# Optimization experiments

Measured on AMD Instinct MI355X. Metric: run time of the kernel, lower is better.

Reference implementation:

```python
import jax, jax.numpy as jnp
import numpy as np

B, N, C = 4, 4096, 1024
NUM_HEADS = 16
HEAD_DIM = C // NUM_HEADS


def setup_inputs() -> dict:
    key = jax.random.key(0)
    k1, k2, k3, k4 = jax.random.split(key, 4)
    s_in = 1.0 / np.sqrt(C)
    return {
        "x": jax.random.normal(k1, (B, N, C), dtype=jnp.float32),
        "H": 64,
        "W": 64,
        "Wqkv": jax.random.normal(k2, (3 * C, C), dtype=jnp.float32) * s_in,
        "Wproj": jax.random.normal(k3, (C, C), dtype=jnp.float32) * s_in,
        "bproj": jnp.zeros((C,), dtype=jnp.float32),
        "alpha": jnp.ones((NUM_HEADS,), dtype=jnp.float32),
    }


def reference(x, H, W, Wqkv, Wproj, bproj, alpha):
    Bb, Nn, Cc = x.shape
    h, d = NUM_HEADS, HEAD_DIM
    # qkv: [B, N, 3C] -> [3, B, h, N, d]
    qkv = jnp.einsum('bnc,oc->bno', x, Wqkv)
    qkv = qkv.reshape(Bb, Nn, 3, h, d).transpose(2, 0, 3, 1, 4)
    q, k, v = qkv[0], qkv[1], qkv[2]  # each [B, h, N, d]
    # channel attention: contract over tokens N -> [B, h, d, d]
    attn = jnp.einsum('bhnd,bhne->bhde', k, q) / alpha[None, :, None, None]
    attn = jax.nn.softmax(attn, axis=-1)
    # (dropout is identity in eval/reference mode)
    # head_out: [B, h, d, N] -> transpose -> [B, N, h, d] -> concat heads
    out = jnp.einsum('bhde,bhne->bhdn', attn, v)
    out = out.transpose(0, 3, 1, 2).reshape(Bb, Nn, Cc)
    return jnp.einsum('bnc,oc->bno', out, Wproj) + bproj
```

## Files before the change

### kernel.cpp

```cpp
#include <hip/hip_runtime.h>
#include <hip/hip_bf16.h>
#include <cstdint>
#include <cstddef>

typedef unsigned short u16;
typedef __bf16 bf16x8 __attribute__((ext_vector_type(8)));
typedef float f32x4 __attribute__((ext_vector_type(4)));
typedef unsigned short u16x4 __attribute__((ext_vector_type(4)));

#define AS1(p) ((__attribute__((address_space(1))) void*)(p))
#define AS3(p) ((__attribute__((address_space(3))) void*)(p))

__device__ __forceinline__ float bf2f(u16 u) {
  unsigned v = ((unsigned)u) << 16; float f; __builtin_memcpy(&f, &v, 4); return f;
}
__device__ __forceinline__ u16 f2bf(float f) {
  unsigned u; __builtin_memcpy(&u, &f, 4);
  u += 0x7FFFu + ((u >> 16) & 1u);
  return (u16)(u >> 16);
}

__global__ __launch_bounds__(256) void convert_kernel(const float* __restrict__ src,
                                                      u16* __restrict__ dst, int n4) {
  int i = blockIdx.x * blockDim.x + threadIdx.x;
  int stride = gridDim.x * blockDim.x;
  for (; i < n4; i += stride) {
    float4 v = ((const float4*)src)[i];
    u16x4 o;
    o.x = f2bf(v.x); o.y = f2bf(v.y); o.z = f2bf(v.z); o.w = f2bf(v.w);
    ((u16x4*)dst)[i] = o;
  }
}

__global__ __launch_bounds__(256) void convert_split_kernel(const float* __restrict__ src,
                                                            u16* __restrict__ hi,
                                                            u16* __restrict__ lo, int n4) {
  int i = blockIdx.x * blockDim.x + threadIdx.x;
  int stride = gridDim.x * blockDim.x;
  for (; i < n4; i += stride) {
    float4 v = ((const float4*)src)[i];
    u16x4 oh, ol;
    oh.x = f2bf(v.x); ol.x = f2bf(v.x - bf2f(oh.x));
    oh.y = f2bf(v.y); ol.y = f2bf(v.y - bf2f(oh.y));
    oh.z = f2bf(v.z); ol.z = f2bf(v.z - bf2f(oh.z));
    oh.w = f2bf(v.w); ol.w = f2bf(v.w - bf2f(oh.w));
    ((u16x4*)hi)[i] = oh;
    ((u16x4*)lo)[i] = ol;
  }
}

__global__ __launch_bounds__(256) void transpose_split_kernel(const float* __restrict__ x,
                                                              u16* __restrict__ Xb,
                                                              u16* __restrict__ XThi,
                                                              u16* __restrict__ XTlo) {
  __shared__ u16 lhi[64 * 68];
  __shared__ u16 llo[64 * 68];
  const int t  = threadIdx.x;
  const int nT = blockIdx.x, cT = blockIdx.y, b = blockIdx.z;
  const size_t xbase = ((size_t)b * 4096 + nT * 64) * 1024 + cT * 64;
  const int c4 = (t & 15) * 4;
  const int r0 = t >> 4;
#pragma unroll
  for (int j = 0; j < 4; ++j) {
    int r = r0 + j * 16;
    float4 v = *(const float4*)(x + xbase + (size_t)r * 1024 + c4);
    u16x4 hi;
    hi.x = f2bf(v.x); hi.y = f2bf(v.y); hi.z = f2bf(v.z); hi.w = f2bf(v.w);
    *(u16x4*)(Xb + xbase + (size_t)r * 1024 + c4) = hi;
    u16 lo[4];
    lo[0] = f2bf(v.x - bf2f(hi.x)); lo[1] = f2bf(v.y - bf2f(hi.y));
    lo[2] = f2bf(v.z - bf2f(hi.z)); lo[3] = f2bf(v.w - bf2f(hi.w));
    u16 hia[4] = { hi.x, hi.y, hi.z, hi.w };
#pragma unroll
    for (int i = 0; i < 4; ++i) {
      lhi[(c4 + i) * 68 + r] = hia[i];
      llo[(c4 + i) * 68 + r] = lo[i];
    }
  }
  __syncthreads();
  const int c  = t >> 2;
  const int n0 = (t & 3) * 16;
  const size_t tbase = ((size_t)b * 1024 + cT * 64 + c) * 4096 + nT * 64 + n0;
#pragma unroll
  for (int q = 0; q < 4; ++q) {
    *(u16x4*)(XThi + tbase + q * 4) = *(const u16x4*)(lhi + c * 68 + n0 + q * 4);
    *(u16x4*)(XTlo + tbase + q * 4) = *(const u16x4*)(llo + c * 68 + n0 + q * 4);
  }
}

template<bool OUT_BF16, bool HAS_BIAS>
__global__ __launch_bounds__(256) void gemm_bt(const u16* __restrict__ A,
                                               const u16* __restrict__ B,
                                               void* __restrict__ Cv,
                                               const float* __restrict__ bias,
                                               int M, int N, int K) {
  __shared__ __align__(16) u16 lA[128 * 32];
  __shared__ __align__(16) u16 lB[128 * 32];
  const int tid  = threadIdx.x;
  const int lane = tid & 63;
  const int wave = tid >> 6;
  const int rowTile = blockIdx.x * 128;
  const int colTile = blockIdx.y * 128;
  const int wr = (wave >> 1) * 64;
  const int wc = (wave & 1) * 64;

  f32x4 acc[4][4] = {};
  const int m  = lane & 15;
  const int ko = (lane >> 4) * 8;

  for (int kt = 0; kt < K; kt += 32) {
#pragma unroll
    for (int i = 0; i < 2; ++i) {
      int idx = i * 256 + tid;
      int row = idx >> 2;
      int kc  = (idx & 3) * 8;
      int ldsOff = (i * 256 + (tid & 192)) * 16;
      __builtin_amdgcn_global_load_lds(AS1(A + (size_t)(rowTile + row) * K + kt + kc),
                                       AS3((char*)lA + ldsOff), 16, 0, 0);
      __builtin_amdgcn_global_load_lds(AS1(B + (size_t)(colTile + row) * K + kt + kc),
                                       AS3((char*)lB + ldsOff), 16, 0, 0);
    }
    __syncthreads();
    bf16x8 af[4], bfr[4];
#pragma unroll
    for (int rb = 0; rb < 4; ++rb)
      af[rb] = *(const bf16x8*)(lA + (wr + rb * 16 + m) * 32 + ko);
#pragma unroll
    for (int cb = 0; cb < 4; ++cb)
      bfr[cb] = *(const bf16x8*)(lB + (wc + cb * 16 + m) * 32 + ko);
#pragma unroll
    for (int rb = 0; rb < 4; ++rb)
#pragma unroll
      for (int cb = 0; cb < 4; ++cb)
        acc[rb][cb] = __builtin_amdgcn_mfma_f32_16x16x32_bf16(af[rb], bfr[cb], acc[rb][cb], 0, 0, 0);
    __syncthreads();
  }

  const int crow0 = rowTile + wr + (lane >> 4) * 4;
  const int ccol0 = colTile + wc + (lane & 15);
#pragma unroll
  for (int rb = 0; rb < 4; ++rb) {
#pragma unroll
    for (int cb = 0; cb < 4; ++cb) {
      int col = ccol0 + cb * 16;
      float bv = HAS_BIAS ? bias[col] : 0.f;
#pragma unroll
      for (int r = 0; r < 4; ++r) {
        int row = crow0 + rb * 16 + r;
        float v = acc[rb][cb][r] + bv;
        if (OUT_BF16) ((u16*)Cv)[(size_t)row * N + col] = f2bf(v);
        else          ((float*)Cv)[(size_t)row * N + col] = v;
      }
    }
  }
}

__global__ __launch_bounds__(256) void gemm_vm(const u16* __restrict__ V,
                                               const u16* __restrict__ Mb,
                                               float* __restrict__ Y,
                                               const float* __restrict__ bias) {
  __shared__ __align__(16) u16 lA[128 * 32];
  __shared__ __align__(16) u16 lB[128 * 32];
  const int tid  = threadIdx.x;
  const int lane = tid & 63;
  const int wave = tid >> 6;
  const int rowTile = blockIdx.x * 128;
  const int colTile = blockIdx.y * 128;
  const int bz = blockIdx.z;
  const u16* A = V + ((size_t)bz << 22);
  const u16* B = Mb + ((size_t)bz << 20);
  float* C = Y + ((size_t)bz << 22);
  const int wr = (wave >> 1) * 64;
  const int wc = (wave & 1) * 64;

  f32x4 acc[4][4] = {};
  const int m  = lane & 15;
  const int ko = (lane >> 4) * 8;

  for (int kt = 0; kt < 1024; kt += 32) {
#pragma unroll
    for (int i = 0; i < 2; ++i) {
      int idx = i * 256 + tid;
      int row = idx >> 2;
      int kc  = (idx & 3) * 8;
      int ldsOff = (i * 256 + (tid & 192)) * 16;
      __builtin_amdgcn_global_load_lds(AS1(A + (size_t)(rowTile + row) * 1024 + kt + kc),
                                       AS3((char*)lA + ldsOff), 16, 0, 0);
      __builtin_amdgcn_global_load_lds(AS1(B + (size_t)(colTile + row) * 1024 + kt + kc),
                                       AS3((char*)lB + ldsOff), 16, 0, 0);
    }
    __syncthreads();
    bf16x8 af[4], bfr[4];
#pragma unroll
    for (int rb = 0; rb < 4; ++rb)
      af[rb] = *(const bf16x8*)(lA + (wr + rb * 16 + m) * 32 + ko);
#pragma unroll
    for (int cb = 0; cb < 4; ++cb)
      bfr[cb] = *(const bf16x8*)(lB + (wc + cb * 16 + m) * 32 + ko);
#pragma unroll
    for (int rb = 0; rb < 4; ++rb)
#pragma unroll
      for (int cb = 0; cb < 4; ++cb)
        acc[rb][cb] = __builtin_amdgcn_mfma_f32_16x16x32_bf16(af[rb], bfr[cb], acc[rb][cb], 0, 0, 0);
    __syncthreads();
  }

  const int crow0 = rowTile + wr + (lane >> 4) * 4;
  const int ccol0 = colTile + wc + (lane & 15);
#pragma unroll
  for (int rb = 0; rb < 4; ++rb)
#pragma unroll
    for (int cb = 0; cb < 4; ++cb) {
      int col = ccol0 + cb * 16;
      float bv = bias[col];
#pragma unroll
      for (int r = 0; r < 4; ++r)
        C[(size_t)(crow0 + rb * 16 + r) * 1024 + col] = acc[rb][cb][r] + bv;
    }
}

__global__ __launch_bounds__(256) void gemm_gram(const u16* __restrict__ XThi,
                                                 const u16* __restrict__ XTlo,
                                                 float* __restrict__ Gpart) {
  __shared__ __align__(16) u16 lAh[128 * 32];
  __shared__ __align__(16) u16 lAl[128 * 32];
  __shared__ __align__(16) u16 lBh[128 * 32];
  __shared__ __align__(16) u16 lBl[128 * 32];
  const int tid  = threadIdx.x;
  const int lane = tid & 63;
  const int wave = tid >> 6;
  const int wr = (wave >> 1) * 64;
  const int wc = (wave & 1) * 64;
  const int m  = lane & 15;
  const int ko = (lane >> 4) * 8;

  const int u0 = blockIdx.x * 36;
  const int b  = u0 / 4608;
  int ub   = u0 - b * 4608;
  int tile = ub >> 7;
  int koff = ub & 127;

  const u16* Ahp = XThi + ((size_t)b << 22);
  const u16* Alp = XTlo + ((size_t)b << 22);
  float* out = Gpart + ((size_t)b << 20);

  int remaining = 36;
  for (int seg = 0; seg < 2 && remaining > 0; ++seg) {
    int niter = min(remaining, 128 - koff);
    int t = tile, rt = 0;
    while (t >= 8 - rt) { t -= 8 - rt; ++rt; }
    int ct = rt + t;
    const int rowTile = rt * 128, colTile = ct * 128;

    f32x4 acc[4][4] = {};
    const int kend = (koff + niter) * 32;
    for (int kt = koff * 32; kt < kend; kt += 32) {
#pragma unroll
      for (int i = 0; i < 2; ++i) {
        int idx = i * 256 + tid;
        int row = idx >> 2;
        int kc  = (idx & 3) * 8;
        int ldsOff = (i * 256 + (tid & 192)) * 16;
        size_t aoff = (size_t)(rowTile + row) * 4096 + kt + kc;
        size_t boff = (size_t)(colTile + row) * 4096 + kt + kc;
        __builtin_amdgcn_global_load_lds(AS1(Ahp + aoff), AS3((char*)lAh + ldsOff), 16, 0, 0);
        __builtin_amdgcn_global_load_lds(AS1(Alp + aoff), AS3((char*)lAl + ldsOff), 16, 0, 0);
        __builtin_amdgcn_global_load_lds(AS1(Ahp + boff), AS3((char*)lBh + ldsOff), 16, 0, 0);
        __builtin_amdgcn_global_load_lds(AS1(Alp + boff), AS3((char*)lBl + ldsOff), 16, 0, 0);
      }
      __syncthreads();
      bf16x8 ah[4], al[4], bh[4], bl[4];
#pragma unroll
      for (int rb = 0; rb < 4; ++rb) {
        ah[rb] = *(const bf16x8*)(lAh + (wr + rb * 16 + m) * 32 + ko);
        al[rb] = *(const bf16x8*)(lAl + (wr + rb * 16 + m) * 32 + ko);
      }
#pragma unroll
      for (int cb = 0; cb < 4; ++cb) {
        bh[cb] = *(const bf16x8*)(lBh + (wc + cb * 16 + m) * 32 + ko);
        bl[cb] = *(const bf16x8*)(lBl + (wc + cb * 16 + m) * 32 + ko);
      }
#pragma unroll
      for (int rb = 0; rb < 4; ++rb)
#pragma unroll
        for (int cb = 0; cb < 4; ++cb) {
          acc[rb][cb] = __builtin_amdgcn_mfma_f32_16x16x32_bf16(ah[rb], bh[cb], acc[rb][cb], 0, 0, 0);
          acc[rb][cb] = __builtin_amdgcn_mfma_f32_16x16x32_bf16(ah[rb], bl[cb], acc[rb][cb], 0, 0, 0);
          acc[rb][cb] = __builtin_amdgcn_mfma_f32_16x16x32_bf16(al[rb], bh[cb], acc[rb][cb], 0, 0, 0);
        }
      __syncthreads();
    }

    const int crow0 = rowTile + wr + (lane >> 4) * 4;
    const int ccol0 = colTile + wc + (lane & 15);
#pragma unroll
    for (int rb = 0; rb < 4; ++rb)
#pragma unroll
      for (int cb = 0; cb < 4; ++cb)
#pragma unroll
        for (int r = 0; r < 4; ++r)
          atomicAdd(&out[(size_t)(crow0 + rb * 16 + r) * 1024 + ccol0 + cb * 16],
                    acc[rb][cb][r]);

    remaining -= niter;
    tile += 1;
    koff = 0;
  }
}

__global__ __launch_bounds__(256) void gram_reduce_split(const float* __restrict__ Gp,
                                                         u16* __restrict__ Ghi,
                                                         u16* __restrict__ Glo) {
  const int rt = blockIdx.x, ct = blockIdx.y, b = blockIdx.z;
  const float* P = Gp + ((size_t)b << 20);
  const bool mirror = (rt >> 1) > (ct >> 1);
  __shared__ float lT[64 * 68];
  const int t = threadIdx.x;
  const int r = t >> 2;
  const int c16 = (t & 3) * 16;

  if (mirror) {
    const size_t bb = (size_t)(ct * 64 + r) * 1024 + rt * 64 + c16;
#pragma unroll
    for (int q = 0; q < 4; ++q)
      *(float4*)(lT + r * 68 + c16 + q * 4) = *(const float4*)(P + bb + q * 4);
    __syncthreads();
  }

  const size_t ab = (size_t)(rt * 64 + r) * 1024 + ct * 64 + c16;
  const size_t ob = ((size_t)b << 20) + ab;
#pragma unroll
  for (int q = 0; q < 4; ++q) {
    float g[4];
    if (mirror) {
#pragma unroll
      for (int i = 0; i < 4; ++i) g[i] = lT[(c16 + q * 4 + i) * 68 + r];
    } else {
      float4 v = *(const float4*)(P + ab + q * 4);
      g[0] = v.x; g[1] = v.y; g[2] = v.z; g[3] = v.w;
    }
    u16x4 oh, ol;
    oh.x = f2bf(g[0]); ol.x = f2bf(g[0] - bf2f(oh.x));
    oh.y = f2bf(g[1]); ol.y = f2bf(g[1] - bf2f(oh.y));
    oh.z = f2bf(g[2]); ol.z = f2bf(g[2] - bf2f(oh.z));
    oh.w = f2bf(g[3]); ol.w = f2bf(g[3] - bf2f(oh.w));
    *(u16x4*)(Ghi + ob + q * 4) = oh;
    *(u16x4*)(Glo + ob + q * 4) = ol;
  }
}

__global__ __launch_bounds__(256) void gemm_tprime(const u16* __restrict__ Wqh,
                                                   const u16* __restrict__ Wql,
                                                   const u16* __restrict__ Ghi,
                                                   const u16* __restrict__ Glo,
                                                   u16* __restrict__ Tph,
                                                   u16* __restrict__ Tpl) {
  __shared__ __align__(16) u16 lAh[128 * 32];
  __shared__ __align__(16) u16 lAl[128 * 32];
  __shared__ __align__(16) u16 lBh[128 * 32];
  __shared__ __align__(16) u16 lBl[128 * 32];
  const int tid  = threadIdx.x;
  const int lane = tid & 63;
  const int wave = tid >> 6;
  const int rowTile = blockIdx.x * 128;
  const int colTile = blockIdx.y * 128;
  const size_t zoff = (size_t)blockIdx.z << 20;
  const int wr = (wave >> 1) * 64;
  const int wc = (wave & 1) * 64;

  f32x4 acc[4][4] = {};
  const int m  = lane & 15;
  const int ko = (lane >> 4) * 8;

  for (int kt = 0; kt < 1024; kt += 32) {
#pragma unroll
    for (int i = 0; i < 2; ++i) {
      int idx = i * 256 + tid;
      int row = idx >> 2;
      int kc  = (idx & 3) * 8;
      int ldsOff = (i * 256 + (tid & 192)) * 16;
      size_t aoff = (size_t)(rowTile + row) * 1024 + kt + kc;
      size_t boff = zoff + (size_t)(colTile + row) * 1024 + kt + kc;
      __builtin_amdgcn_global_load_lds(AS1(Wqh + aoff), AS3((char*)lAh + ldsOff), 16, 0, 0);
      __builtin_amdgcn_global_load_lds(AS1(Wql + aoff), AS3((char*)lAl + ldsOff), 16, 0, 0);
      __builtin_amdgcn_global_load_lds(AS1(Ghi + boff), AS3((char*)lBh + ldsOff), 16, 0, 0);
      __builtin_amdgcn_global_load_lds(AS1(Glo + boff), AS3((char*)lBl + ldsOff), 16, 0, 0);
    }
    __syncthreads();
    bf16x8 ah[4], al[4], bh[4], bl[4];
#pragma unroll
    for (int rb = 0; rb < 4; ++rb) {
      ah[rb] = *(const bf16x8*)(lAh + (wr + rb * 16 + m) * 32 + ko);
      al[rb] = *(const bf16x8*)(lAl + (wr + rb * 16 + m) * 32 + ko);
    }
#pragma unroll
    for (int cb = 0; cb < 4; ++cb) {
      bh[cb] = *(const bf16x8*)(lBh + (wc + cb * 16 + m) * 32 + ko);
      bl[cb] = *(const bf16x8*)(lBl + (wc + cb * 16 + m) * 32 + ko);
    }
#pragma unroll
    for (int rb = 0; rb < 4; ++rb)
#pragma unroll
      for (int cb = 0; cb < 4; ++cb) {
        acc[rb][cb] = __builtin_amdgcn_mfma_f32_16x16x32_bf16(ah[rb], bh[cb], acc[rb][cb], 0, 0, 0);
        acc[rb][cb] = __builtin_amdgcn_mfma_f32_16x16x32_bf16(ah[rb], bl[cb], acc[rb][cb], 0, 0, 0);
        acc[rb][cb] = __builtin_amdgcn_mfma_f32_16x16x32_bf16(al[rb], bh[cb], acc[rb][cb], 0, 0, 0);
      }
    __syncthreads();
  }

  const int crow0 = rowTile + wr + (lane >> 4) * 4;
  const int ccol0 = colTile + wc + (lane & 15);
#pragma unroll
  for (int rb = 0; rb < 4; ++rb)
#pragma unroll
    for (int cb = 0; cb < 4; ++cb)
#pragma unroll
      for (int r = 0; r < 4; ++r) {
        float v = acc[rb][cb][r];
        u16 hi = f2bf(v);
        u16 lo = f2bf(v - bf2f(hi));
        size_t off = zoff + (size_t)(crow0 + rb * 16 + r) * 1024 + ccol0 + cb * 16;
        Tph[off] = hi;
        Tpl[off] = lo;
      }
}

__global__ __launch_bounds__(256) void s_softmax_kernel(const u16* __restrict__ Wqh,
                                                        const u16* __restrict__ Wql,
                                                        const u16* __restrict__ Tph,
                                                        const u16* __restrict__ Tpl,
                                                        const float* __restrict__ alpha,
                                                        u16* __restrict__ attnT) {
  const int h = blockIdx.x, b = blockIdx.y;
  const int tid = threadIdx.x, lane = tid & 63, wave = tid >> 6;
  __shared__ __align__(16) u16 lAh[64 * 32];
  __shared__ __align__(16) u16 lAl[64 * 32];
  __shared__ __align__(16) u16 lBh[64 * 32];
  __shared__ __align__(16) u16 lBl[64 * 32];

  const size_t aBase = (size_t)(1024 + h * 64) * 1024;
  const size_t bBase = ((size_t)b << 20) + (size_t)(h * 64) * 1024;

  f32x4 acc[4] = {};
  const int m  = lane & 15;
  const int ko = (lane >> 4) * 8;
  const int srow = tid >> 2;
  const int skc  = (tid & 3) * 8;
  const int ldsOff = (tid & 192) * 16;

  for (int kt = 0; kt < 1024; kt += 32) {
    __builtin_amdgcn_global_load_lds(AS1(Wqh + aBase + (size_t)srow * 1024 + kt + skc),
                                     AS3((char*)lAh + ldsOff), 16, 0, 0);
    __builtin_amdgcn_global_load_lds(AS1(Wql + aBase + (size_t)srow * 1024 + kt + skc),
                                     AS3((char*)lAl + ldsOff), 16, 0, 0);
    __builtin_amdgcn_global_load_lds(AS1(Tph + bBase + (size_t)srow * 1024 + kt + skc),
                                     AS3((char*)lBh + ldsOff), 16, 0, 0);
    __builtin_amdgcn_global_load_lds(AS1(Tpl + bBase + (size_t)srow * 1024 + kt + skc),
                                     AS3((char*)lBl + ldsOff), 16, 0, 0);
    __syncthreads();
    bf16x8 ah = *(const bf16x8*)(lAh + (wave * 16 + m) * 32 + ko);
    bf16x8 al = *(const bf16x8*)(lAl + (wave * 16 + m) * 32 + ko);
#pragma unroll
    for (int cb = 0; cb < 4; ++cb) {
      bf16x8 bh = *(const bf16x8*)(lBh + (cb * 16 + m) * 32 + ko);
      bf16x8 bl = *(const bf16x8*)(lBl + (cb * 16 + m) * 32 + ko);
      acc[cb] = __builtin_amdgcn_mfma_f32_16x16x32_bf16(ah, bh, acc[cb], 0, 0, 0);
      acc[cb] = __builtin_amdgcn_mfma_f32_16x16x32_bf16(ah, bl, acc[cb], 0, 0, 0);
      acc[cb] = __builtin_amdgcn_mfma_f32_16x16x32_bf16(al, bh, acc[cb], 0, 0, 0);
    }
    __syncthreads();
  }

  const float invA = 1.f / alpha[h];
  const int g = lane >> 4;
  const size_t obase = (size_t)(b * 16 + h) * 4096;
#pragma unroll
  for (int r = 0; r < 4; ++r) {
    int d = wave * 16 + g * 4 + r;
    float s[4];
#pragma unroll
    for (int cb = 0; cb < 4; ++cb) s[cb] = acc[cb][r] * invA;
    float mx = fmaxf(fmaxf(s[0], s[1]), fmaxf(s[2], s[3]));
#pragma unroll
    for (int o = 1; o < 16; o <<= 1) mx = fmaxf(mx, __shfl_xor(mx, o, 64));
    float e[4]; float sum = 0.f;
#pragma unroll
    for (int cb = 0; cb < 4; ++cb) { e[cb] = __expf(s[cb] - mx); sum += e[cb]; }
#pragma unroll
    for (int o = 1; o < 16; o <<= 1) sum += __shfl_xor(sum, o, 64);
    float inv = 1.f / sum;
#pragma unroll
    for (int cb = 0; cb < 4; ++cb) {
      int e_idx = cb * 16 + (lane & 15);
      attnT[obase + (size_t)e_idx * 64 + d] = f2bf(e[cb] * inv);
    }
  }
}

__global__ __launch_bounds__(256) void m_build_kernel(const u16* __restrict__ Wpb,
                                                      const u16* __restrict__ attnT,
                                                      u16* __restrict__ Mb) {
  const int oT = blockIdx.x, h = blockIdx.y, b = blockIdx.z;
  const int tid = threadIdx.x, lane = tid & 63, wave = tid >> 6;
  __shared__ __align__(16) u16 lA[128 * 64];
  __shared__ __align__(16) u16 lB[64 * 64];
  const int bh = b * 16 + h;
#pragma unroll
  for (int i = 0; i < 4; ++i) {
    int idx = i * 256 + tid;
    int row = idx >> 3;
    int kc  = (idx & 7) * 8;
    int ldsOff = (i * 256 + (tid & 192)) * 16;
    __builtin_amdgcn_global_load_lds(AS1(Wpb + (size_t)(oT * 128 + row) * 1024 + h * 64 + kc),
                                     AS3((char*)lA + ldsOff), 16, 0, 0);
  }
#pragma unroll
  for (int i = 0; i < 2; ++i) {
    int idx = i * 256 + tid;
    int ldsOff = (i * 256 + (tid & 192)) * 16;
    __builtin_amdgcn_global_load_lds(AS1(attnT + (size_t)bh * 4096 + idx * 8),
                                     AS3((char*)lB + ldsOff), 16, 0, 0);
  }
  __syncthreads();
  const int m  = lane & 15;
  const int ko = (lane >> 4) * 8;
  const int wr = wave * 32;
  f32x4 acc[2][4] = {};
#pragma unroll
  for (int ks = 0; ks < 2; ++ks) {
#pragma unroll
    for (int rb = 0; rb < 2; ++rb) {
      bf16x8 a = *(const bf16x8*)(lA + (wr + rb * 16 + m) * 64 + ks * 32 + ko);
#pragma unroll
      for (int cb = 0; cb < 4; ++cb) {
        bf16x8 bb = *(const bf16x8*)(lB + (cb * 16 + m) * 64 + ks * 32 + ko);
        acc[rb][cb] = __builtin_amdgcn_mfma_f32_16x16x32_bf16(a, bb, acc[rb][cb], 0, 0, 0);
      }
    }
  }
  u16* out = Mb + ((size_t)b << 20);
#pragma unroll
  for (int rb = 0; rb < 2; ++rb)
#pragma unroll
    for (int cb = 0; cb < 4; ++cb) {
      int col = h * 64 + cb * 16 + (lane & 15);
#pragma unroll
      for (int r = 0; r < 4; ++r) {
        int row = oT * 128 + wr + rb * 16 + (lane >> 4) * 4 + r;
        out[(size_t)row * 1024 + col] = f2bf(acc[rb][cb][r]);
      }
    }
}

extern "C" void kernel_launch(void* const* d_in, const int* in_sizes, int n_in,
                              void* d_out, int out_size, void* d_ws, size_t ws_size,
                              hipStream_t stream) {
  const float* x     = (const float*)d_in[0];
  const float* Wqkv  = (const float*)d_in[3];
  const float* Wproj = (const float*)d_in[4];
  const float* bproj = (const float*)d_in[5];
  const float* alpha = (const float*)d_in[6];

  char* ws = (char*)d_ws;
  u16*   Xb     = (u16*)ws;
  float* Gpart  = (float*)ws;
  u16*   Mb     = (u16*)ws;
  u16*   XThi   = (u16*)(ws + 33554432);
  u16*   attnTb = (u16*)(ws + 33554432);
  u16*   XTlo  = (u16*)(ws + 67108864);
  u16*   Ghi   = (u16*)(ws + 67108864);
  u16*   Glo   = (u16*)(ws + 75497472);
  u16*   Tph   = (u16*)(ws + 83886080);
  u16*   Tpl   = (u16*)(ws + 92274688);
  u16*   Wqh   = (u16*)(ws + 100663296);
  u16*   Wql   = (u16*)(ws + 106954752);
  u16*   Vb    = (u16*)(ws + 113246208);
  u16*   Wpb   = (u16*)(ws + 146800640);

  transpose_split_kernel<<<dim3(64, 16, 4), 256, 0, stream>>>(x, Xb, XThi, XTlo);
  convert_split_kernel<<<256, 256, 0, stream>>>(Wqkv, Wqh, Wql, 3145728 / 4);
  convert_kernel<<<128, 256, 0, stream>>>(Wproj, Wpb, 1048576 / 4);
  gemm_bt<true, false><<<dim3(128, 8), 256, 0, stream>>>(
      Xb, Wqh + (size_t)2048 * 1024, Vb, nullptr, 16384, 1024, 1024);
  hipMemsetAsync(Gpart, 0, (size_t)4 * 1024 * 1024 * 4, stream);
  gemm_gram<<<512, 256, 0, stream>>>(XThi, XTlo, Gpart);
  gram_reduce_split<<<dim3(16, 16, 4), 256, 0, stream>>>(Gpart, Ghi, Glo);
  gemm_tprime<<<dim3(8, 8, 4), 256, 0, stream>>>(Wqh, Wql, Ghi, Glo, Tph, Tpl);
  s_softmax_kernel<<<dim3(16, 4), 256, 0, stream>>>(Wqh, Wql, Tph, Tpl, alpha, attnTb);
  m_build_kernel<<<dim3(8, 16, 4), 256, 0, stream>>>(Wpb, attnTb, Mb);
  gemm_vm<<<dim3(32, 8, 4), 256, 0, stream>>>(Vb, Mb, (float*)d_out, bproj);
}
```

Baseline: 458.5 us.

## Restructure Gram GEMM split-K into fixed quarter slices with plain stores

The Gram kernel no longer assigns each block a flat run of 36 k-iterations that may span two tiles. It now uses a 2D grid where each upper-triangle tile is split into four K quarters. For off-diagonal tiles, the two upper quarters are written transposed into the mirror position, so each output location gets plain stores instead of atomics. Diagonal tiles still accumulate with atomics into two slice buffers, and the reduce kernel now sums both slices plus the mirrored transpose. This removes most atomic traffic and the segment bookkeeping, at the cost of a larger memset and extra partial-buffer reads in the reduce.

```diff
diff --git a/kernel.cpp b/kernel.cpp
--- a/kernel.cpp
+++ b/kernel.cpp
@@ -234,65 +234,64 @@
   const int m  = lane & 15;
   const int ko = (lane >> 4) * 8;
 
-  const int u0 = blockIdx.x * 36;
-  const int b  = u0 / 4608;
-  int ub   = u0 - b * 4608;
-  int tile = ub >> 7;
-  int koff = ub & 127;
+  const int jx = blockIdx.x;
+  const int b  = blockIdx.y;
+  const int tile = jx >> 2, kq = jx & 3;
+  int t = tile, rt = 0;
+  while (t >= 8 - rt) { t -= 8 - rt; ++rt; }
+  const int ct = rt + t;
+  const bool diag = (rt == ct);
+  int rT = rt, cT = ct;
+  if (!diag && kq >= 2) { rT = ct; cT = rt; }
+  const int slice = kq & 1;
+  const int rowTile = rT * 128, colTile = cT * 128;
+  const int k0 = kq * 1024;
 
   const u16* Ahp = XThi + ((size_t)b << 22);
   const u16* Alp = XTlo + ((size_t)b << 22);
-  float* out = Gpart + ((size_t)b << 20);
-
-  int remaining = 36;
-  for (int seg = 0; seg < 2 && remaining > 0; ++seg) {
-    int niter = min(remaining, 128 - koff);
-    int t = tile, rt = 0;
-    while (t >= 8 - rt) { t -= 8 - rt; ++rt; }
-    int ct = rt + t;
-    const int rowTile = rt * 128, colTile = ct * 128;
-
-    f32x4 acc[4][4] = {};
-    const int kend = (koff + niter) * 32;
-    for (int kt = koff * 32; kt < kend; kt += 32) {
-#pragma unroll
-      for (int i = 0; i < 2; ++i) {
-        int idx = i * 256 + tid;
-        int row = idx >> 2;
-        int kc  = (idx & 3) * 8;
-        int ldsOff = (i * 256 + (tid & 192)) * 16;
-        size_t aoff = (size_t)(rowTile + row) * 4096 + kt + kc;
-        size_t boff = (size_t)(colTile + row) * 4096 + kt + kc;
-        __builtin_amdgcn_global_load_lds(AS1(Ahp + aoff), AS3((char*)lAh + ldsOff), 16, 0, 0);
-        __builtin_amdgcn_global_load_lds(AS1(Alp + aoff), AS3((char*)lAl + ldsOff), 16, 0, 0);
-        __builtin_amdgcn_global_load_lds(AS1(Ahp + boff), AS3((char*)lBh + ldsOff), 16, 0, 0);
-        __builtin_amdgcn_global_load_lds(AS1(Alp + boff), AS3((char*)lBl + ldsOff), 16, 0, 0);
+
+  f32x4 acc[4][4] = {};
+  for (int kt = k0; kt < k0 + 1024; kt += 32) {
+#pragma unroll
+    for (int i = 0; i < 2; ++i) {
+      int idx = i * 256 + tid;
+      int row = idx >> 2;
+      int kc  = (idx & 3) * 8;
+      int ldsOff = (i * 256 + (tid & 192)) * 16;
+      size_t aoff = (size_t)(rowTile + row) * 4096 + kt + kc;
+      size_t boff = (size_t)(colTile + row) * 4096 + kt + kc;
+      __builtin_amdgcn_global_load_lds(AS1(Ahp + aoff), AS3((char*)lAh + ldsOff), 16, 0, 0);
+      __builtin_amdgcn_global_load_lds(AS1(Alp + aoff), AS3((char*)lAl + ldsOff), 16, 0, 0);
+      __builtin_amdgcn_global_load_lds(AS1(Ahp + boff), AS3((char*)lBh + ldsOff), 16, 0, 0);
+      __builtin_amdgcn_global_load_lds(AS1(Alp + boff), AS3((char*)lBl + ldsOff), 16, 0, 0);
+    }
+    __syncthreads();
+    bf16x8 ah[4], al[4], bh[4], bl[4];
+#pragma unroll
+    for (int rb = 0; rb < 4; ++rb) {
+      ah[rb] = *(const bf16x8*)(lAh + (wr + rb * 16 + m) * 32 + ko);
+      al[rb] = *(const bf16x8*)(lAl + (wr + rb * 16 + m) * 32 + ko);
+    }
+#pragma unroll
+    for (int cb = 0; cb < 4; ++cb) {
+      bh[cb] = *(const bf16x8*)(lBh + (wc + cb * 16 + m) * 32 + ko);
+      bl[cb] = *(const bf16x8*)(lBl + (wc + cb * 16 + m) * 32 + ko);
+    }
+#pragma unroll
+    for (int rb = 0; rb < 4; ++rb)
+#pragma unroll
+      for (int cb = 0; cb < 4; ++cb) {
+        acc[rb][cb] = __builtin_amdgcn_mfma_f32_16x16x32_bf16(ah[rb], bh[cb], acc[rb][cb], 0, 0, 0);
+        acc[rb][cb] = __builtin_amdgcn_mfma_f32_16x16x32_bf16(ah[rb], bl[cb], acc[rb][cb], 0, 0, 0);
+        acc[rb][cb] = __builtin_amdgcn_mfma_f32_16x16x32_bf16(al[rb], bh[cb], acc[rb][cb], 0, 0, 0);
       }
-      __syncthreads();
-      bf16x8 ah[4], al[4], bh[4], bl[4];
-#pragma unroll
-      for (int rb = 0; rb < 4; ++rb) {
-        ah[rb] = *(const bf16x8*)(lAh + (wr + rb * 16 + m) * 32 + ko);
-        al[rb] = *(const bf16x8*)(lAl + (wr + rb * 16 + m) * 32 + ko);
-      }
-#pragma unroll
-      for (int cb = 0; cb < 4; ++cb) {
-        bh[cb] = *(const bf16x8*)(lBh + (wc + cb * 16 + m) * 32 + ko);
-        bl[cb] = *(const bf16x8*)(lBl + (wc + cb * 16 + m) * 32 + ko);
-      }
-#pragma unroll
-      for (int rb = 0; rb < 4; ++rb)
-#pragma unroll
-        for (int cb = 0; cb < 4; ++cb) {
-          acc[rb][cb] = __builtin_amdgcn_mfma_f32_16x16x32_bf16(ah[rb], bh[cb], acc[rb][cb], 0, 0, 0);
-          acc[rb][cb] = __builtin_amdgcn_mfma_f32_16x16x32_bf16(ah[rb], bl[cb], acc[rb][cb], 0, 0, 0);
-          acc[rb][cb] = __builtin_amdgcn_mfma_f32_16x16x32_bf16(al[rb], bh[cb], acc[rb][cb], 0, 0, 0);
-        }
-      __syncthreads();
-    }
-
-    const int crow0 = rowTile + wr + (lane >> 4) * 4;
-    const int ccol0 = colTile + wc + (lane & 15);
+    __syncthreads();
+  }
+
+  float* out = Gpart + ((size_t)(slice * 4 + b) << 20);
+  const int crow0 = rowTile + wr + (lane >> 4) * 4;
+  const int ccol0 = colTile + wc + (lane & 15);
+  if (diag) {
 #pragma unroll
     for (int rb = 0; rb < 4; ++rb)
 #pragma unroll
@@ -301,10 +300,14 @@
         for (int r = 0; r < 4; ++r)
           atomicAdd(&out[(size_t)(crow0 + rb * 16 + r) * 1024 + ccol0 + cb * 16],
                     acc[rb][cb][r]);
-
-    remaining -= niter;
-    tile += 1;
-    koff = 0;
+  } else {
+#pragma unroll
+    for (int rb = 0; rb < 4; ++rb)
+#pragma unroll
+      for (int cb = 0; cb < 4; ++cb)
+#pragma unroll
+        for (int r = 0; r < 4; ++r)
+          out[(size_t)(crow0 + rb * 16 + r) * 1024 + ccol0 + cb * 16] = acc[rb][cb][r];
   }
 }
 
@@ -312,18 +315,23 @@
                                                          u16* __restrict__ Ghi,
                                                          u16* __restrict__ Glo) {
   const int rt = blockIdx.x, ct = blockIdx.y, b = blockIdx.z;
-  const float* P = Gp + ((size_t)b << 20);
-  const bool mirror = (rt >> 1) > (ct >> 1);
+  const bool diag128 = (rt >> 1) == (ct >> 1);
+  const float* s0 = Gp + ((size_t)b << 20);
+  const float* s1 = Gp + ((size_t)(4 + b) << 20);
   __shared__ float lT[64 * 68];
   const int t = threadIdx.x;
   const int r = t >> 2;
   const int c16 = (t & 3) * 16;
 
-  if (mirror) {
+  if (!diag128) {
     const size_t bb = (size_t)(ct * 64 + r) * 1024 + rt * 64 + c16;
 #pragma unroll
-    for (int q = 0; q < 4; ++q)
-      *(float4*)(lT + r * 68 + c16 + q * 4) = *(const float4*)(P + bb + q * 4);
+    for (int q = 0; q < 4; ++q) {
+      float4 v0 = *(const float4*)(s0 + bb + q * 4);
+      float4 v1 = *(const float4*)(s1 + bb + q * 4);
+      float4 s = { v0.x + v1.x, v0.y + v1.y, v0.z + v1.z, v0.w + v1.w };
+      *(float4*)(lT + r * 68 + c16 + q * 4) = s;
+    }
     __syncthreads();
   }
 
@@ -331,13 +339,12 @@
   const size_t ob = ((size_t)b << 20) + ab;
 #pragma unroll
   for (int q = 0; q < 4; ++q) {
-    float g[4];
-    if (mirror) {
-#pragma unroll
-      for (int i = 0; i < 4; ++i) g[i] = lT[(c16 + q * 4 + i) * 68 + r];
-    } else {
-      float4 v = *(const float4*)(P + ab + q * 4);
-      g[0] = v.x; g[1] = v.y; g[2] = v.z; g[3] = v.w;
+    float4 v0 = *(const float4*)(s0 + ab + q * 4);
+    float4 v1 = *(const float4*)(s1 + ab + q * 4);
+    float g[4] = { v0.x + v1.x, v0.y + v1.y, v0.z + v1.z, v0.w + v1.w };
+    if (!diag128) {
+#pragma unroll
+      for (int i = 0; i < 4; ++i) g[i] += lT[(c16 + q * 4 + i) * 68 + r];
     }
     u16x4 oh, ol;
     oh.x = f2bf(g[0]); ol.x = f2bf(g[0] - bf2f(oh.x));
@@ -583,8 +590,8 @@
   convert_kernel<<<128, 256, 0, stream>>>(Wproj, Wpb, 1048576 / 4);
   gemm_bt<true, false><<<dim3(128, 8), 256, 0, stream>>>(
       Xb, Wqh + (size_t)2048 * 1024, Vb, nullptr, 16384, 1024, 1024);
-  hipMemsetAsync(Gpart, 0, (size_t)4 * 1024 * 1024 * 4, stream);
-  gemm_gram<<<512, 256, 0, stream>>>(XThi, XTlo, Gpart);
+  hipMemsetAsync(Gpart, 0, (size_t)33554432, stream);
+  gemm_gram<<<dim3(144, 4), 256, 0, stream>>>(XThi, XTlo, Gpart);
   gram_reduce_split<<<dim3(16, 16, 4), 256, 0, stream>>>(Gpart, Ghi, Glo);
   gemm_tprime<<<dim3(8, 8, 4), 256, 0, stream>>>(Wqh, Wql, Ghi, Glo, Tph, Tpl);
   s_softmax_kernel<<<dim3(16, 4), 256, 0, stream>>>(Wqh, Wql, Tph, Tpl, alpha, attnTb);
```

New measurement: 440.2 us. 1.04x faster.
